# Kernel tuning notes

Measured on AMD Instinct MI355X. Metric: run time of the kernel, lower is better.

Reference implementation:

```python
import jax, jax.numpy as jnp
import numpy as np

N, NODE_F, EDGE_F = 50000, 192, 64
M = 800000  # directed edges
D = NODE_F + EDGE_F  # inner_dim = 256
OUT = 2048
DEPTH = 3


def setup_inputs() -> dict:
    key = jax.random.key(0)
    ks = jax.random.split(key, 8)
    node_attr = jax.random.normal(ks[0], (N, NODE_F), dtype=jnp.float32)
    edge_attr = jax.random.normal(ks[1], (M, EDGE_F), dtype=jnp.float32)
    edge_src = jax.random.randint(ks[2], (M,), 0, N, dtype=jnp.int32)
    edge_dst = jax.random.randint(ks[3], (M,), 0, N, dtype=jnp.int32)
    # per-depth parameters (original stacks copies along a depth axis)
    W_inner = jnp.stack([jnp.eye(D, dtype=jnp.float32)
                         + 0.01 * jax.random.normal(jax.random.fold_in(ks[4], d), (D, D))
                         for d in range(DEPTH)])                      # [DEPTH, D, D]
    b_inner = jnp.zeros((DEPTH, D), dtype=jnp.float32)
    scale = jnp.sqrt(6.0 / (D + OUT)).astype(jnp.float32)            # glorot_uniform
    W_output = jax.random.uniform(ks[5], (DEPTH + 1, D, OUT), jnp.float32, -scale, scale)
    b_output = jnp.zeros((DEPTH + 1, OUT), dtype=jnp.float32)
    return {"node_attr": node_attr, "edge_attr": edge_attr,
            "edge_src": edge_src, "edge_dst": edge_dst,
            "W_inner": W_inner, "b_inner": b_inner,
            "W_output": W_output, "b_output": b_output}


def _fp_contribution(attr, W_out_d, b_out_d):
    # softmax over fingerprint dim per node, summed over nodes -> [OUT]
    return jax.nn.softmax(attr @ W_out_d + b_out_d, axis=-1).sum(axis=0)


def reference(node_attr, edge_attr, edge_src, edge_dst,
              W_inner, b_inner, W_output, b_output):
    n = node_attr.shape[0]
    # attributes = [nodeAttributes | zeros(edge_feat)]  -> [N, D]
    attr = jnp.concatenate(
        [node_attr, jnp.zeros((n, edge_attr.shape[1]), node_attr.dtype)], axis=1)
    fp = _fp_contribution(attr, W_output[0], b_output[0])
    # per-edge payload: [zeros(node_feat) | edgeAttr]  -> [M, D]
    edge_pad = jnp.concatenate(
        [jnp.zeros((edge_attr.shape[0], node_attr.shape[1]), edge_attr.dtype), edge_attr],
        axis=1)
    for d in range(1, DEPTH + 1):
        # v_i = attr_i + sum_{(ni,ei) in nbrs(i)} (attr_ni + [0|edgeAttr_ei])
        msgs = attr[edge_src] + edge_pad                 # [M, D] gather
        agg = jax.ops.segment_sum(msgs, edge_dst, num_segments=n)
        v = attr + agg
        # activation_inner = 'linear' (identity)
        attr = v @ W_inner[d - 1] + b_inner[d - 1]
        fp = fp + _fp_contribution(attr, W_output[d], b_output[d])
    return fp  # [OUT]
```

## Files before the change

### kernel.cpp

```cpp
#include <hip/hip_runtime.h>
#include <hip/hip_bf16.h>

#define N_NODES 50000
#define N_PAD   50016
#define NODE_F  192
#define EDGE_F  64
#define DIM     256
#define OUT_DIM 2048
#define DEPTH   3
#define M_EDGES 800000

typedef short  bf16x8 __attribute__((ext_vector_type(8)));
typedef float  f32x4  __attribute__((ext_vector_type(4)));

__device__ inline short f2bf(float f) {
    unsigned u = __float_as_uint(f);
    unsigned r = (u + 0x7fffu + ((u >> 16) & 1u)) >> 16;
    return (short)r;
}

__global__ void k_init_attr(const float* __restrict__ node_attr,
                            float* __restrict__ attr,
                            short* __restrict__ attr_bf) {
    int i = blockIdx.x * 256 + threadIdx.x;
    int row = i >> 6, q = i & 63;
    if (row >= N_PAD) return;
    float4 v = make_float4(0.f, 0.f, 0.f, 0.f);
    if (row < N_NODES && q < NODE_F / 4)
        v = ((const float4*)node_attr)[row * (NODE_F / 4) + q];
    if (row < N_NODES) ((float4*)attr)[i] = v;
    short4 s; s.x = f2bf(v.x); s.y = f2bf(v.y); s.z = f2bf(v.z); s.w = f2bf(v.w);
    ((short4*)attr_bf)[i] = s;
}

__global__ void k_degree(const int* __restrict__ dst, int* __restrict__ deg) {
    int e = blockIdx.x * 256 + threadIdx.x;
    if (e < M_EDGES) atomicAdd(&deg[dst[e]], 1);
}

__global__ __launch_bounds__(1024) void k_scan(int* __restrict__ deg,
                                               int* __restrict__ rowptr) {
    __shared__ int part[1024];
    int t = threadIdx.x;
    const int CH = (N_NODES + 1023) / 1024;
    int beg = t * CH, end = min(beg + CH, N_NODES);
    int s = 0;
    for (int i = beg; i < end; i++) s += deg[i];
    part[t] = s;
    __syncthreads();
    for (int off = 1; off < 1024; off <<= 1) {
        int v = (t >= off) ? part[t - off] : 0;
        __syncthreads();
        part[t] += v;
        __syncthreads();
    }
    int run = (t == 0) ? 0 : part[t - 1];
    for (int i = beg; i < end; i++) {
        int d = deg[i];
        rowptr[i] = run;
        deg[i] = run;
        run += d;
    }
    if (t == 1023) rowptr[N_NODES] = run;
}

__global__ void k_fill(const int* __restrict__ dst, const int* __restrict__ src,
                       int* __restrict__ cursor,
                       int* __restrict__ eidx, int* __restrict__ srcs) {
    int e = blockIdx.x * 256 + threadIdx.x;
    if (e < M_EDGES) {
        int p = atomicAdd(&cursor[dst[e]], 1);
        eidx[p] = e;
        srcs[p] = src[e];
    }
}

__global__ __launch_bounds__(256) void k_esum(const float* __restrict__ edge_attr,
                                              const int* __restrict__ rowptr,
                                              const int* __restrict__ eidx,
                                              float* __restrict__ esum) {
    int gid = blockIdx.x * 256 + threadIdx.x;
    int node = gid >> 4, q = gid & 15;
    if (node >= N_NODES) return;
    int beg = rowptr[node], end = rowptr[node + 1];
    float4 acc = make_float4(0.f, 0.f, 0.f, 0.f);
    const float4* E4 = (const float4*)edge_attr;
    for (int i = beg; i < end; i++) {
        int e = eidx[i];
        float4 v = E4[(size_t)e * 16 + q];
        acc.x += v.x; acc.y += v.y; acc.z += v.z; acc.w += v.w;
    }
    ((float4*)esum)[(size_t)node * 16 + q] = acc;
}

__global__ __launch_bounds__(256) void k_gather(const float* __restrict__ attr,
                                                const int* __restrict__ rowptr,
                                                const int* __restrict__ srcs,
                                                const float* __restrict__ esum,
                                                float* __restrict__ agg) {
    int gid = blockIdx.x * 256 + threadIdx.x;
    int node = gid >> 6, q = gid & 63;
    if (node >= N_NODES) return;
    int beg = rowptr[node], end = rowptr[node + 1];
    float4 acc = make_float4(0.f, 0.f, 0.f, 0.f);
    if (q >= NODE_F / 4)
        acc = ((const float4*)esum)[(size_t)node * 16 + (q - NODE_F / 4)];
    const float4* A4 = (const float4*)attr;
    for (int i = beg; i < end; i++) {
        int s = srcs[i];
        float4 v = A4[(size_t)s * 64 + q];
        acc.x += v.x; acc.y += v.y; acc.z += v.z; acc.w += v.w;
    }
    ((float4*)agg)[(size_t)node * 64 + q] = acc;
}

__global__ __launch_bounds__(256) void k_inner(const float* __restrict__ attr,
                                               const float* __restrict__ agg,
                                               const float* __restrict__ W,
                                               const float* __restrict__ b,
                                               float* __restrict__ out,
                                               short* __restrict__ out_bf) {
    __shared__ float4 sV[32][64];
    int tid  = threadIdx.x;
    int row0 = blockIdx.x * 32;

    for (int i = tid; i < 32 * 64; i += 256) {
        int r = i >> 6, q = i & 63;
        int grow = row0 + r;
        float4 v = make_float4(0.f, 0.f, 0.f, 0.f);
        if (grow < N_NODES) {
            float4 a = ((const float4*)attr)[(size_t)grow * 64 + q];
            float4 g = ((const float4*)agg)[(size_t)grow * 64 + q];
            v = make_float4(a.x + g.x, a.y + g.y, a.z + g.z, a.w + g.w);
        }
        sV[r][q] = v;
    }
    __syncthreads();

    int cg = tid & 63;
    int rg = tid >> 6;

    float4 acc[8];
#pragma unroll
    for (int r = 0; r < 8; r++) acc[r] = make_float4(0.f, 0.f, 0.f, 0.f);

    const float4* W4 = (const float4*)W;
    for (int k4 = 0; k4 < 64; k4++) {
        float4 w0 = W4[(size_t)(k4 * 4 + 0) * 64 + cg];
        float4 w1 = W4[(size_t)(k4 * 4 + 1) * 64 + cg];
        float4 w2 = W4[(size_t)(k4 * 4 + 2) * 64 + cg];
        float4 w3 = W4[(size_t)(k4 * 4 + 3) * 64 + cg];
#pragma unroll
        for (int r = 0; r < 8; r++) {
            float4 a = sV[rg * 8 + r][k4];
            acc[r].x += a.x * w0.x + a.y * w1.x + a.z * w2.x + a.w * w3.x;
            acc[r].y += a.x * w0.y + a.y * w1.y + a.z * w2.y + a.w * w3.y;
            acc[r].z += a.x * w0.z + a.y * w1.z + a.z * w2.z + a.w * w3.z;
            acc[r].w += a.x * w0.w + a.y * w1.w + a.z * w2.w + a.w * w3.w;
        }
    }

    float4 bb = ((const float4*)b)[cg];
#pragma unroll
    for (int r = 0; r < 8; r++) {
        int grow = row0 + rg * 8 + r;
        if (grow < N_NODES) {
            float4 o = make_float4(acc[r].x + bb.x, acc[r].y + bb.y,
                                   acc[r].z + bb.z, acc[r].w + bb.w);
            ((float4*)out)[(size_t)grow * 64 + cg] = o;
            short4 s; s.x = f2bf(o.x); s.y = f2bf(o.y); s.z = f2bf(o.z); s.w = f2bf(o.w);
            ((short4*)out_bf)[(size_t)grow * 64 + cg] = s;
        }
    }
}

__global__ void k_wswz(const float* __restrict__ W, short* __restrict__ Wz) {
    int idx = blockIdx.x * 256 + threadIdx.x;
    int lane = idx & 63;
    int T    = (idx >> 6) & 127;
    int ks   = (idx >> 13) & 7;
    int d    = idx >> 16;
    int quad = lane >> 4;
    int m    = lane & 15;
    const float* src = W + ((size_t)(d * 256 + ks * 32 + quad * 8)) * 2048 + T * 16 + m;
    short* dstp = Wz + (size_t)idx * 8;
#pragma unroll
    for (int j = 0; j < 8; j++) dstp[j] = f2bf(src[(size_t)j * 2048]);
}

__global__ __launch_bounds__(1024)
void k_fp_mfma(const short* __restrict__ attr_bf,
               const short* __restrict__ Wz,
               const float* __restrict__ bias,
               float* __restrict__ fp_part) {
    __shared__ float sred[32][17];
    __shared__ float sfinm[32];
    __shared__ float sfinl[32];
    int tid  = threadIdx.x;
    int lane = tid & 63;
    int wave = tid >> 6;
    int quad = lane >> 4;
    int m    = lane & 15;
    int row0 = blockIdx.x * 32;

    f32x4 acc0[8], acc1[8];
#pragma unroll
    for (int t = 0; t < 8; t++) {
        acc0[t] = (f32x4){0.f, 0.f, 0.f, 0.f};
        acc1[t] = (f32x4){0.f, 0.f, 0.f, 0.f};
    }

    const short* a0p = attr_bf + (size_t)(row0 + m) * 256 + quad * 8;
    const short* a1p = a0p + 16 * 256;
    for (int ks = 0; ks < 8; ks++) {
        bf16x8 af0 = *(const bf16x8*)(a0p + ks * 32);
        bf16x8 af1 = *(const bf16x8*)(a1p + ks * 32);
        const bf16x8* bp = (const bf16x8*)Wz + ((size_t)ks * 128 + wave * 8) * 64 + lane;
#pragma unroll
        for (int t = 0; t < 8; t++) {
            bf16x8 bf = bp[t * 64];
            acc0[t] = __builtin_amdgcn_mfma_f32_16x16x32_bf16(af0, bf, acc0[t], 0, 0, 0);
            acc1[t] = __builtin_amdgcn_mfma_f32_16x16x32_bf16(af1, bf, acc1[t], 0, 0, 0);
        }
    }

#pragma unroll
    for (int t = 0; t < 8; t++) {
        float bb = bias[(wave * 8 + t) * 16 + m];
        acc0[t][0] += bb; acc0[t][1] += bb; acc0[t][2] += bb; acc0[t][3] += bb;
        acc1[t][0] += bb; acc1[t][1] += bb; acc1[t][2] += bb; acc1[t][3] += bb;
    }

    float mx0[4], mx1[4];
#pragma unroll
    for (int r = 0; r < 4; r++) {
        float v0 = acc0[0][r], v1 = acc1[0][r];
#pragma unroll
        for (int t = 1; t < 8; t++) { v0 = fmaxf(v0, acc0[t][r]); v1 = fmaxf(v1, acc1[t][r]); }
        mx0[r] = v0; mx1[r] = v1;
    }
#pragma unroll
    for (int off = 1; off < 16; off <<= 1)
#pragma unroll
        for (int r = 0; r < 4; r++) {
            mx0[r] = fmaxf(mx0[r], __shfl_xor(mx0[r], off));
            mx1[r] = fmaxf(mx1[r], __shfl_xor(mx1[r], off));
        }
    if (m == 0)
#pragma unroll
        for (int r = 0; r < 4; r++) {
            sred[quad * 4 + r][wave]      = mx0[r];
            sred[16 + quad * 4 + r][wave] = mx1[r];
        }
    __syncthreads();
    if (tid < 32) {
        float v = sred[tid][0];
#pragma unroll
        for (int w = 1; w < 16; w++) v = fmaxf(v, sred[tid][w]);
        sfinm[tid] = v;
    }
    __syncthreads();
#pragma unroll
    for (int r = 0; r < 4; r++) { mx0[r] = sfinm[quad * 4 + r]; mx1[r] = sfinm[16 + quad * 4 + r]; }

    float ls0[4] = {0.f, 0.f, 0.f, 0.f}, ls1[4] = {0.f, 0.f, 0.f, 0.f};
#pragma unroll
    for (int t = 0; t < 8; t++) {
#pragma unroll
        for (int r = 0; r < 4; r++) {
            float e0 = __expf(acc0[t][r] - mx0[r]);
            float e1 = __expf(acc1[t][r] - mx1[r]);
            acc0[t][r] = e0; acc1[t][r] = e1;
            ls0[r] += e0; ls1[r] += e1;
        }
    }
#pragma unroll
    for (int off = 1; off < 16; off <<= 1)
#pragma unroll
        for (int r = 0; r < 4; r++) {
            ls0[r] += __shfl_xor(ls0[r], off);
            ls1[r] += __shfl_xor(ls1[r], off);
        }
    if (m == 0)
#pragma unroll
        for (int r = 0; r < 4; r++) {
            sred[quad * 4 + r][wave]      = ls0[r];
            sred[16 + quad * 4 + r][wave] = ls1[r];
        }
    __syncthreads();
    if (tid < 32) {
        float v = 0.f;
#pragma unroll
        for (int w = 0; w < 16; w++) v += sred[tid][w];
        sfinl[tid] = v;
    }
    __syncthreads();

    float rinv0[4], rinv1[4];
#pragma unroll
    for (int r = 0; r < 4; r++) {
        int ra = quad * 4 + r, rb = 16 + quad * 4 + r;
        rinv0[r] = (row0 + ra < N_NODES) ? 1.0f / sfinl[ra] : 0.0f;
        rinv1[r] = (row0 + rb < N_NODES) ? 1.0f / sfinl[rb] : 0.0f;
    }

    float* dst = fp_part + (size_t)(blockIdx.x & 63) * OUT_DIM;
#pragma unroll
    for (int t = 0; t < 8; t++) {
        float cs = acc0[t][0] * rinv0[0] + acc0[t][1] * rinv0[1]
                 + acc0[t][2] * rinv0[2] + acc0[t][3] * rinv0[3]
                 + acc1[t][0] * rinv1[0] + acc1[t][1] * rinv1[1]
                 + acc1[t][2] * rinv1[2] + acc1[t][3] * rinv1[3];
        cs += __shfl_xor(cs, 16);
        cs += __shfl_xor(cs, 32);
        if (quad == 0)
            atomicAdd(&dst[(wave * 8 + t) * 16 + m], cs);
    }
}

__global__ void k_fp_reduce(const float* __restrict__ part, float* __restrict__ fp) {
    int c = blockIdx.x * 256 + threadIdx.x;
    float s = 0.f;
#pragma unroll
    for (int r = 0; r < 64; r++) s += part[(size_t)r * OUT_DIM + c];
    fp[c] = s;
}

extern "C" void kernel_launch(void* const* d_in, const int* in_sizes, int n_in,
                              void* d_out, int out_size, void* d_ws, size_t ws_size,
                              hipStream_t stream) {
    const float* node_attr = (const float*)d_in[0];
    const float* edge_attr = (const float*)d_in[1];
    const int*   edge_src  = (const int*)d_in[2];
    const int*   edge_dst  = (const int*)d_in[3];
    const float* W_inner   = (const float*)d_in[4];
    const float* b_inner   = (const float*)d_in[5];
    const float* W_output  = (const float*)d_in[6];
    const float* b_output  = (const float*)d_in[7];

    float* fp      = (float*)d_out;
    float* attr    = (float*)d_ws;
    float* agg     = attr + (size_t)N_NODES * DIM;
    float* fp_part = agg + (size_t)N_NODES * DIM;
    short* Wz      = (short*)(fp_part + 64 * OUT_DIM);
    int*   deg     = (int*)(Wz + (size_t)4 * 65536 * 8);
    int*   rowptr  = deg + N_NODES;
    int*   eidx    = rowptr + N_NODES + 1;
    int*   srcs    = eidx + M_EDGES;
    float* esum    = (float*)(srcs + M_EDGES);
    short* attr_bf = (short*)(esum + (size_t)N_NODES * EDGE_F);

    hipMemsetAsync(fp_part, 0, 64 * OUT_DIM * sizeof(float), stream);
    hipMemsetAsync(deg, 0, N_NODES * sizeof(int), stream);

    k_init_attr<<<(N_PAD * 64 + 255) / 256, 256, 0, stream>>>(node_attr, attr, attr_bf);

    k_degree<<<(M_EDGES + 255) / 256, 256, 0, stream>>>(edge_dst, deg);
    k_scan<<<1, 1024, 0, stream>>>(deg, rowptr);
    k_fill<<<(M_EDGES + 255) / 256, 256, 0, stream>>>(edge_dst, edge_src, deg, eidx, srcs);
    k_esum<<<(N_NODES * 16 + 255) / 256, 256, 0, stream>>>(edge_attr, rowptr, eidx, esum);

    k_wswz<<<1024, 256, 0, stream>>>(W_output, Wz);

    k_fp_mfma<<<N_PAD / 32, 1024, 0, stream>>>(attr_bf, Wz, b_output, fp_part);

    for (int d = 1; d <= DEPTH; d++) {
        k_gather<<<(N_NODES * 64 + 255) / 256, 256, 0, stream>>>(
            attr, rowptr, srcs, esum, agg);
        k_inner<<<(N_NODES + 31) / 32, 256, 0, stream>>>(
            attr, agg, W_inner + (size_t)(d - 1) * DIM * DIM,
            b_inner + (size_t)(d - 1) * DIM, attr, attr_bf);
        k_fp_mfma<<<N_PAD / 32, 1024, 0, stream>>>(
            attr_bf, Wz + (size_t)d * 65536 * 8,
            b_output + (size_t)d * OUT_DIM, fp_part);
    }
    k_fp_reduce<<<OUT_DIM / 256, 256, 0, stream>>>(fp_part, fp);
}
```

Before: 1.867 ms.

## Stage A tile in LDS, reorder swizzled weights, fuse residual into gather, enlarge inner tile

k_fp_mfma now copies the 32-row bf16 activation tile into XOR-swizzled LDS via global_load_lds. The output weights are re-laid out so each wave streams contiguous B fragments, with a staggered k-start per block/wave and s_setprio around the MFMA groups. The gather kernel folds attr+esum into its accumulator and unrolls neighbour loads by four with independent partial sums, so k_inner reads a single input and now processes 64 rows per block with 16 accumulators per thread. Partial fp buffers drop from 64 to 32, which adds atomic contention; the larger k_inner register footprint may lower occupancy.

```diff
diff --git a/kernel.cpp b/kernel.cpp
--- a/kernel.cpp
+++ b/kernel.cpp
@@ -18,6 +18,12 @@
     unsigned r = (u + 0x7fffu + ((u >> 16) & 1u)) >> 16;
     return (short)r;
 }
+
+#define GLDS16(g, l) __builtin_amdgcn_global_load_lds(                        \
+    (const __attribute__((address_space(1))) void*)(g),                       \
+    (__attribute__((address_space(3))) void*)(l), 16, 0, 0)
+
+#define MFMA16(a, b, c) __builtin_amdgcn_mfma_f32_16x16x32_bf16((a), (b), (c), 0, 0, 0)
 
 __global__ void k_init_attr(const float* __restrict__ node_attr,
                             float* __restrict__ attr,
@@ -97,42 +103,56 @@
                                                 const int* __restrict__ rowptr,
                                                 const int* __restrict__ srcs,
                                                 const float* __restrict__ esum,
-                                                float* __restrict__ agg) {
+                                                float* __restrict__ v_out) {
     int gid = blockIdx.x * 256 + threadIdx.x;
     int node = gid >> 6, q = gid & 63;
     if (node >= N_NODES) return;
     int beg = rowptr[node], end = rowptr[node + 1];
-    float4 acc = make_float4(0.f, 0.f, 0.f, 0.f);
-    if (q >= NODE_F / 4)
-        acc = ((const float4*)esum)[(size_t)node * 16 + (q - NODE_F / 4)];
     const float4* A4 = (const float4*)attr;
-    for (int i = beg; i < end; i++) {
-        int s = srcs[i];
-        float4 v = A4[(size_t)s * 64 + q];
-        acc.x += v.x; acc.y += v.y; acc.z += v.z; acc.w += v.w;
-    }
-    ((float4*)agg)[(size_t)node * 64 + q] = acc;
-}
-
-__global__ __launch_bounds__(256) void k_inner(const float* __restrict__ attr,
-                                               const float* __restrict__ agg,
+    float4 acc = A4[(size_t)node * 64 + q];
+    if (q >= NODE_F / 4) {
+        float4 e = ((const float4*)esum)[(size_t)node * 16 + (q - NODE_F / 4)];
+        acc.x += e.x; acc.y += e.y; acc.z += e.z; acc.w += e.w;
+    }
+    float4 s0 = make_float4(0.f, 0.f, 0.f, 0.f), s1 = s0, s2 = s0, s3 = s0;
+    int i = beg;
+    for (; i + 4 <= end; i += 4) {
+        int n0 = srcs[i], n1 = srcs[i + 1], n2 = srcs[i + 2], n3 = srcs[i + 3];
+        float4 v0 = A4[(size_t)n0 * 64 + q];
+        float4 v1 = A4[(size_t)n1 * 64 + q];
+        float4 v2 = A4[(size_t)n2 * 64 + q];
+        float4 v3 = A4[(size_t)n3 * 64 + q];
+        s0.x += v0.x; s0.y += v0.y; s0.z += v0.z; s0.w += v0.w;
+        s1.x += v1.x; s1.y += v1.y; s1.z += v1.z; s1.w += v1.w;
+        s2.x += v2.x; s2.y += v2.y; s2.z += v2.z; s2.w += v2.w;
+        s3.x += v3.x; s3.y += v3.y; s3.z += v3.z; s3.w += v3.w;
+    }
+    for (; i < end; i++) {
+        float4 v0 = A4[(size_t)srcs[i] * 64 + q];
+        s0.x += v0.x; s0.y += v0.y; s0.z += v0.z; s0.w += v0.w;
+    }
+    acc.x += s0.x + s1.x + s2.x + s3.x;
+    acc.y += s0.y + s1.y + s2.y + s3.y;
+    acc.z += s0.z + s1.z + s2.z + s3.z;
+    acc.w += s0.w + s1.w + s2.w + s3.w;
+    ((float4*)v_out)[(size_t)node * 64 + q] = acc;
+}
+
+__global__ __launch_bounds__(256) void k_inner(const float* __restrict__ v_in,
                                                const float* __restrict__ W,
                                                const float* __restrict__ b,
                                                float* __restrict__ out,
                                                short* __restrict__ out_bf) {
-    __shared__ float4 sV[32][64];
+    __shared__ float4 sV[64][64];
     int tid  = threadIdx.x;
-    int row0 = blockIdx.x * 32;
-
-    for (int i = tid; i < 32 * 64; i += 256) {
+    int row0 = blockIdx.x * 64;
+
+    for (int i = tid; i < 64 * 64; i += 256) {
         int r = i >> 6, q = i & 63;
         int grow = row0 + r;
         float4 v = make_float4(0.f, 0.f, 0.f, 0.f);
-        if (grow < N_NODES) {
-            float4 a = ((const float4*)attr)[(size_t)grow * 64 + q];
-            float4 g = ((const float4*)agg)[(size_t)grow * 64 + q];
-            v = make_float4(a.x + g.x, a.y + g.y, a.z + g.z, a.w + g.w);
-        }
+        if (grow < N_NODES)
+            v = ((const float4*)v_in)[(size_t)grow * 64 + q];
         sV[r][q] = v;
     }
     __syncthreads();
@@ -140,9 +160,9 @@
     int cg = tid & 63;
     int rg = tid >> 6;
 
-    float4 acc[8];
-#pragma unroll
-    for (int r = 0; r < 8; r++) acc[r] = make_float4(0.f, 0.f, 0.f, 0.f);
+    float4 acc[16];
+#pragma unroll
+    for (int r = 0; r < 16; r++) acc[r] = make_float4(0.f, 0.f, 0.f, 0.f);
 
     const float4* W4 = (const float4*)W;
     for (int k4 = 0; k4 < 64; k4++) {
@@ -151,8 +171,8 @@
         float4 w2 = W4[(size_t)(k4 * 4 + 2) * 64 + cg];
         float4 w3 = W4[(size_t)(k4 * 4 + 3) * 64 + cg];
 #pragma unroll
-        for (int r = 0; r < 8; r++) {
-            float4 a = sV[rg * 8 + r][k4];
+        for (int r = 0; r < 16; r++) {
+            float4 a = sV[rg * 16 + r][k4];
             acc[r].x += a.x * w0.x + a.y * w1.x + a.z * w2.x + a.w * w3.x;
             acc[r].y += a.x * w0.y + a.y * w1.y + a.z * w2.y + a.w * w3.y;
             acc[r].z += a.x * w0.z + a.y * w1.z + a.z * w2.z + a.w * w3.z;
@@ -162,8 +182,8 @@
 
     float4 bb = ((const float4*)b)[cg];
 #pragma unroll
-    for (int r = 0; r < 8; r++) {
-        int grow = row0 + rg * 8 + r;
+    for (int r = 0; r < 16; r++) {
+        int grow = row0 + rg * 16 + r;
         if (grow < N_NODES) {
             float4 o = make_float4(acc[r].x + bb.x, acc[r].y + bb.y,
                                    acc[r].z + bb.z, acc[r].w + bb.w);
@@ -183,9 +203,11 @@
     int quad = lane >> 4;
     int m    = lane & 15;
     const float* src = W + ((size_t)(d * 256 + ks * 32 + quad * 8)) * 2048 + T * 16 + m;
-    short* dstp = Wz + (size_t)idx * 8;
-#pragma unroll
-    for (int j = 0; j < 8; j++) dstp[j] = f2bf(src[(size_t)j * 2048]);
+    int w = T >> 3, h = (T >> 2) & 1, j = T & 3;
+    size_t n = ((((size_t)(ks * 2 + h)) * 16 + w) * 4 + j) * 64 + lane;
+    short* dstp = Wz + ((size_t)d * 65536 + n) * 8;
+#pragma unroll
+    for (int jj = 0; jj < 8; jj++) dstp[jj] = f2bf(src[(size_t)jj * 2048]);
 }
 
 __global__ __launch_bounds__(1024)
@@ -193,6 +215,7 @@
                const short* __restrict__ Wz,
                const float* __restrict__ bias,
                float* __restrict__ fp_part) {
+    __shared__ __align__(16) short A_lds[32 * 256];
     __shared__ float sred[32][17];
     __shared__ float sfinm[32];
     __shared__ float sfinl[32];
@@ -202,6 +225,17 @@
     int quad = lane >> 4;
     int m    = lane & 15;
     int row0 = blockIdx.x * 32;
+    int sw   = (m & 7) << 4;
+
+    {
+        int r   = tid >> 5;
+        int c16 = tid & 31;
+        const char* gsrc = (const char*)attr_bf
+            + (size_t)(row0 + r) * 512 + (size_t)((c16 * 16) ^ ((r & 7) << 4));
+        GLDS16(gsrc, (char*)A_lds + (size_t)wave * 1024);
+    }
+    asm volatile("s_waitcnt vmcnt(0)" ::: "memory");
+    __syncthreads();
 
     f32x4 acc0[8], acc1[8];
 #pragma unroll
@@ -210,18 +244,31 @@
         acc1[t] = (f32x4){0.f, 0.f, 0.f, 0.f};
     }
 
-    const short* a0p = attr_bf + (size_t)(row0 + m) * 256 + quad * 8;
-    const short* a1p = a0p + 16 * 256;
-    for (int ks = 0; ks < 8; ks++) {
-        bf16x8 af0 = *(const bf16x8*)(a0p + ks * 32);
-        bf16x8 af1 = *(const bf16x8*)(a1p + ks * 32);
-        const bf16x8* bp = (const bf16x8*)Wz + ((size_t)ks * 128 + wave * 8) * 64 + lane;
-#pragma unroll
-        for (int t = 0; t < 8; t++) {
-            bf16x8 bf = bp[t * 64];
-            acc0[t] = __builtin_amdgcn_mfma_f32_16x16x32_bf16(af0, bf, acc0[t], 0, 0, 0);
-            acc1[t] = __builtin_amdgcn_mfma_f32_16x16x32_bf16(af1, bf, acc1[t], 0, 0, 0);
-        }
+    const bf16x8* Bp = (const bf16x8*)Wz + ((size_t)(wave * 4) * 64 + lane);
+    int start = ((blockIdx.x + wave) & 7) << 1;
+
+    for (int pp = 0; pp < 8; pp++) {
+        int u0 = (start + 2 * pp) & 15;
+        int ks = u0 >> 1;
+        int co = (quad * 16 + ks * 64) ^ sw;
+        bf16x8 af0 = *(const bf16x8*)((const char*)A_lds + m * 512 + co);
+        bf16x8 af1 = *(const bf16x8*)((const char*)A_lds + (m + 16) * 512 + co);
+        const bf16x8* Bu = Bp + (size_t)u0 * 4096;
+        bf16x8 b0 = Bu[0], b1 = Bu[64], b2 = Bu[128], b3 = Bu[192];
+        const bf16x8* Bv = Bu + 4096;
+        bf16x8 c0 = Bv[0], c1 = Bv[64], c2 = Bv[128], c3 = Bv[192];
+        __builtin_amdgcn_s_setprio(1);
+        acc0[0] = MFMA16(af0, b0, acc0[0]);  acc1[0] = MFMA16(af1, b0, acc1[0]);
+        acc0[1] = MFMA16(af0, b1, acc0[1]);  acc1[1] = MFMA16(af1, b1, acc1[1]);
+        acc0[2] = MFMA16(af0, b2, acc0[2]);  acc1[2] = MFMA16(af1, b2, acc1[2]);
+        acc0[3] = MFMA16(af0, b3, acc0[3]);  acc1[3] = MFMA16(af1, b3, acc1[3]);
+        __builtin_amdgcn_s_setprio(0);
+        __builtin_amdgcn_s_setprio(1);
+        acc0[4] = MFMA16(af0, c0, acc0[4]);  acc1[4] = MFMA16(af1, c0, acc1[4]);
+        acc0[5] = MFMA16(af0, c1, acc0[5]);  acc1[5] = MFMA16(af1, c1, acc1[5]);
+        acc0[6] = MFMA16(af0, c2, acc0[6]);  acc1[6] = MFMA16(af1, c2, acc1[6]);
+        acc0[7] = MFMA16(af0, c3, acc0[7]);  acc1[7] = MFMA16(af1, c3, acc1[7]);
+        __builtin_amdgcn_s_setprio(0);
     }
 
 #pragma unroll
@@ -304,7 +351,7 @@
         rinv1[r] = (row0 + rb < N_NODES) ? 1.0f / sfinl[rb] : 0.0f;
     }
 
-    float* dst = fp_part + (size_t)(blockIdx.x & 63) * OUT_DIM;
+    float* dst = fp_part + (size_t)(blockIdx.x & 31) * OUT_DIM;
 #pragma unroll
     for (int t = 0; t < 8; t++) {
         float cs = acc0[t][0] * rinv0[0] + acc0[t][1] * rinv0[1]
@@ -322,7 +369,7 @@
     int c = blockIdx.x * 256 + threadIdx.x;
     float s = 0.f;
 #pragma unroll
-    for (int r = 0; r < 64; r++) s += part[(size_t)r * OUT_DIM + c];
+    for (int r = 0; r < 32; r++) s += part[(size_t)r * OUT_DIM + c];
     fp[c] = s;
 }
 
@@ -342,15 +389,15 @@
     float* attr    = (float*)d_ws;
     float* agg     = attr + (size_t)N_NODES * DIM;
     float* fp_part = agg + (size_t)N_NODES * DIM;
-    short* Wz      = (short*)(fp_part + 64 * OUT_DIM);
+    short* Wz      = (short*)(fp_part + 32 * OUT_DIM);
     int*   deg     = (int*)(Wz + (size_t)4 * 65536 * 8);
     int*   rowptr  = deg + N_NODES;
-    int*   eidx    = rowptr + N_NODES + 1;
+    int*   eidx    = rowptr + N_NODES + 4;
     int*   srcs    = eidx + M_EDGES;
     float* esum    = (float*)(srcs + M_EDGES);
     short* attr_bf = (short*)(esum + (size_t)N_NODES * EDGE_F);
 
-    hipMemsetAsync(fp_part, 0, 64 * OUT_DIM * sizeof(float), stream);
+    hipMemsetAsync(fp_part, 0, 32 * OUT_DIM * sizeof(float), stream);
     hipMemsetAsync(deg, 0, N_NODES * sizeof(int), stream);
 
     k_init_attr<<<(N_PAD * 64 + 255) / 256, 256, 0, stream>>>(node_attr, attr, attr_bf);
@@ -367,8 +414,8 @@
     for (int d = 1; d <= DEPTH; d++) {
         k_gather<<<(N_NODES * 64 + 255) / 256, 256, 0, stream>>>(
             attr, rowptr, srcs, esum, agg);
-        k_inner<<<(N_NODES + 31) / 32, 256, 0, stream>>>(
-            attr, agg, W_inner + (size_t)(d - 1) * DIM * DIM,
+        k_inner<<<(N_NODES + 63) / 64, 256, 0, stream>>>(
+            agg, W_inner + (size_t)(d - 1) * DIM * DIM,
             b_inner + (size_t)(d - 1) * DIM, attr, attr_bf);
         k_fp_mfma<<<N_PAD / 32, 1024, 0, stream>>>(
             attr_bf, Wz + (size_t)d * 65536 * 8,
```

Result: faster. 1.711 ms (-8.3%).
